# Performance work log

Measured on AMD Instinct MI355X. Metric: run time of the kernel, lower is better.

Reference implementation:

```python
import jax, jax.numpy as jnp
import numpy as np

N_HEADS = 16
HEAD_DIM = 128  # dim // n_heads = 2048 // 16

def setup_inputs() -> dict:
    key = jax.random.key(0)
    ks = jax.random.split(key, 7)
    B, S, D = 2, 2048, 2048
    scale = 0.02
    return {
        "q": jax.random.normal(ks[0], (B, S, D), dtype=jnp.float32),
        "k": jax.random.normal(ks[1], (B, S, D), dtype=jnp.float32),
        "v": jax.random.normal(ks[2], (B, S, D), dtype=jnp.float32),
        "wq": jax.random.normal(ks[3], (D, D), dtype=jnp.float32) * scale,
        "wk": jax.random.normal(ks[4], (D, D), dtype=jnp.float32) * scale,
        "wv": jax.random.normal(ks[5], (D, D), dtype=jnp.float32) * scale,
        "wo": jax.random.normal(ks[6], (D, D), dtype=jnp.float32) * scale,
    }

def reference(q, k, v, wq, wk, wv, wo):
    B, S, _ = q.shape
    # Linear (no bias): torch Linear computes x @ W.T; weights here stored as [out, in]
    xq = (q @ wq.T).reshape(B, S, N_HEADS, HEAD_DIM).transpose(0, 2, 1, 3)  # [B,H,S,d]
    xk = (k @ wk.T).reshape(B, S, N_HEADS, HEAD_DIM).transpose(0, 2, 1, 3)
    xv = (v @ wv.T).reshape(B, S, N_HEADS, HEAD_DIM).transpose(0, 2, 1, 3)
    scores = jnp.einsum("bhqd,bhkd->bhqk", xq, xk) / jnp.sqrt(jnp.float32(HEAD_DIM))
    # causal mask: -inf above the diagonal
    causal = jnp.tril(jnp.ones((S, S), dtype=bool))
    scores = jnp.where(causal[None, None], scores, -jnp.inf)
    attn = jax.nn.softmax(scores.astype(jnp.float32), axis=-1)  # dropout is identity at eval
    out = jnp.einsum("bhqk,bhkd->bhqd", attn, xv)
    out = out.transpose(0, 2, 1, 3).reshape(B, S, N_HEADS * HEAD_DIM)
    return out @ wo.T
```

## Files before the change

kernel.cpp:

```cpp
#include <hip/hip_runtime.h>
#include <hip/hip_bf16.h>

#define B_ 2
#define S_ 2048
#define D_ 2048
#define H_ 16
#define HD_ 128

typedef __attribute__((ext_vector_type(4))) float f32x4;
typedef __attribute__((ext_vector_type(8))) short bf16x8;

static __device__ __forceinline__ unsigned short f2bf(float f) {
    unsigned int u = __float_as_uint(f);
    u += 0x7fffu + ((u >> 16) & 1u);
    return (unsigned short)(u >> 16);
}
static __device__ __forceinline__ float bf2f(unsigned short h) {
    return __uint_as_float(((unsigned int)h) << 16);
}

#define MFMA_K32(a, b, c) __builtin_amdgcn_mfma_f32_16x16x32_bf16(a, b, c, 0, 0, 0)

static __device__ __forceinline__ void gll16(const void* g, void* l) {
    __builtin_amdgcn_global_load_lds((const __attribute__((address_space(1))) void*)g,
                                     (__attribute__((address_space(3))) void*)l,
                                     16, 0, 0);
}

__global__ void cvt_in(const float4* __restrict__ src, ushort4* __restrict__ dst) {
    int i = blockIdx.x * 256 + threadIdx.x;
    float4 v = src[i];
    ushort4 o;
    o.x = f2bf(v.x); o.y = f2bf(v.y); o.z = f2bf(v.z); o.w = f2bf(v.w);
    dst[i] = o;
}

__global__ void cvt_w4(const float4* __restrict__ s0, ushort4* __restrict__ d0,
                       const float4* __restrict__ s1, ushort4* __restrict__ d1,
                       const float4* __restrict__ s2, ushort4* __restrict__ d2,
                       const float4* __restrict__ s3, ushort4* __restrict__ d3) {
    const float4* s; ushort4* d;
    switch (blockIdx.y) {
        case 0: s = s0; d = d0; break;
        case 1: s = s1; d = d1; break;
        case 2: s = s2; d = d2; break;
        default: s = s3; d = d3; break;
    }
    int i = blockIdx.x * 256 + threadIdx.x;
    float4 v = s[i];
    ushort4 o;
    o.x = f2bf(v.x); o.y = f2bf(v.y); o.z = f2bf(v.z); o.w = f2bf(v.w);
    d[i] = o;
}

template<int OUT_MODE>
__global__ __launch_bounds__(256) void gemm_xwt(
        const unsigned short* __restrict__ A,
        const unsigned short* __restrict__ W,
        void* __restrict__ C) {
    constexpr int K = D_;
    __shared__ unsigned short As[2][128 * 32];
    __shared__ unsigned short Ws[2][128 * 32];
    const int tid = threadIdx.x, lane = tid & 63, wid = tid >> 6;
    const int wy = wid >> 1, wx = wid & 1;
    const int g = lane >> 4, lr = lane & 15;
    const int swz = (blockIdx.x & 7) * 64 + (blockIdx.x >> 3);
    const int bm = (swz & 31) * 128;
    const int bn = (swz >> 5) * 128;

    const int r0 = (wid * 128 + lane) >> 2, c0 = (lane & 3) * 8;
    const int r1 = r0 + 16;

    f32x4 acc[4][4] = {};

    auto stage = [&](int k0, int nb) {
        gll16(A + (size_t)(bm + r0) * K + k0 + c0, (char*)&As[nb][0] + wid * 2048);
        gll16(A + (size_t)(bm + r1) * K + k0 + c0, (char*)&As[nb][0] + wid * 2048 + 1024);
        gll16(W + (size_t)(bn + r0) * K + k0 + c0, (char*)&Ws[nb][0] + wid * 2048);
        gll16(W + (size_t)(bn + r1) * K + k0 + c0, (char*)&Ws[nb][0] + wid * 2048 + 1024);
    };

    stage(0, 0);
    int cur = 0;

    for (int k0 = 0; k0 < K; k0 += 32) {
        __syncthreads();
        if (k0 + 32 < K) stage(k0 + 32, cur ^ 1);
        bf16x8 af[4], wf[4];
        #pragma unroll
        for (int i = 0; i < 4; ++i)
            af[i] = *(const bf16x8*)((const char*)&As[cur][0] + (wy * 64 + i * 16 + lr) * 64 + g * 16);
        #pragma unroll
        for (int i = 0; i < 4; ++i)
            wf[i] = *(const bf16x8*)((const char*)&Ws[cur][0] + (wx * 64 + i * 16 + lr) * 64 + g * 16);
        #pragma unroll
        for (int mi = 0; mi < 4; ++mi)
            #pragma unroll
            for (int ni = 0; ni < 4; ++ni)
                acc[mi][ni] = MFMA_K32(af[mi], wf[ni], acc[mi][ni]);
        cur ^= 1;
    }

    #pragma unroll
    for (int mi = 0; mi < 4; ++mi) {
        #pragma unroll
        for (int ni = 0; ni < 4; ++ni) {
            const int n = bn + wx * 64 + ni * 16 + lr;
            const int m0 = bm + wy * 64 + mi * 16 + g * 4;
            if constexpr (OUT_MODE == 0) {
                #pragma unroll
                for (int rg = 0; rg < 4; ++rg) {
                    int m = m0 + rg;
                    int bb = m >> 11, s = m & (S_ - 1);
                    int hh = n >> 7, dd = n & (HD_ - 1);
                    ((unsigned short*)C)[(((size_t)(bb * H_ + hh) * S_) + s) * HD_ + dd] =
                        f2bf(acc[mi][ni][rg]);
                }
            } else if constexpr (OUT_MODE == 1) {
                #pragma unroll
                for (int rg = 0; rg < 4; ++rg) {
                    int m = m0 + rg;
                    int bb = m >> 11, s = m & (S_ - 1);
                    int hh = n >> 7, dd = n & (HD_ - 1);
                    int vr = s & 63;
                    int pr = (vr & 3) | (((vr >> 3) & 3) << 2) | (((vr >> 2) & 1) << 4) | (vr & 32);
                    size_t eo = ((size_t)(bb * H_ + hh) << 18) + ((size_t)(s >> 6) << 13)
                              + pr * 128 + (((((unsigned)dd) << 1) ^ ((pr & 7) << 4)) >> 1);
                    ((unsigned short*)C)[eo] = f2bf(acc[mi][ni][rg]);
                }
            } else if constexpr (OUT_MODE == 2) {
                int bb = m0 >> 11, s0 = m0 & (S_ - 1);
                int hh = n >> 7, dd = n & (HD_ - 1);
                int ch = ((s0 & 63) >> 3) ^ (dd & 7);
                size_t eo = ((size_t)(bb * H_ + hh) << 18) + ((size_t)(s0 >> 6) << 13)
                          + dd * 64 + (ch << 3) + (s0 & 7);
                ushort4 pk;
                pk.x = f2bf(acc[mi][ni][0]); pk.y = f2bf(acc[mi][ni][1]);
                pk.z = f2bf(acc[mi][ni][2]); pk.w = f2bf(acc[mi][ni][3]);
                *(ushort4*)&((unsigned short*)C)[eo] = pk;
            } else {
                #pragma unroll
                for (int rg = 0; rg < 4; ++rg)
                    ((float*)C)[(size_t)(m0 + rg) * D_ + n] = acc[mi][ni][rg];
            }
        }
    }
}

__global__ __launch_bounds__(256) void attn_fwd(
        const unsigned short* __restrict__ Qg,
        const unsigned short* __restrict__ Kt,
        const unsigned short* __restrict__ Vt,
        unsigned short* __restrict__ Og) {
    __shared__ char Ks[2][16384];
    __shared__ char Vs[2][16384];
    const int tid = threadIdx.x, lane = tid & 63, w = tid >> 6;
    const int g = lane >> 4, lr = lane & 15;
    const int swz = (blockIdx.x & 7) * 32 + (blockIdx.x >> 3);
    const int bh = swz >> 3, pi = swz & 7;
    const int b = bh >> 4, h = bh & (H_ - 1);
    const size_t base = (size_t)bh * S_ * HD_;
    const float SCL = 0.08838834764831845f * 1.4426950408889634f;

    auto stage = [&](int t, int nb) {
        const size_t tb = base + (size_t)t * 8192 + w * 2048 + (size_t)lane * 8;
        char* kd = &Ks[nb][0] + w * 4096;
        char* vd = &Vs[nb][0] + w * 4096;
        gll16(Kt + tb, kd);        gll16(Kt + tb + 512, kd + 1024);
        gll16(Kt + tb + 1024, kd + 2048); gll16(Kt + tb + 1536, kd + 3072);
        gll16(Vt + tb, vd);        gll16(Vt + tb + 512, vd + 1024);
        gll16(Vt + tb + 1024, vd + 2048); gll16(Vt + tb + 1536, vd + 3072);
    };

    int cur = 0;
    #pragma unroll 1
    for (int half = 0; half < 2; ++half) {
        const int qt = half ? (15 - pi) : pi;
        const int q0 = qt * 128;
        const int qrA = q0 + w * 16 + lr, qrB = qrA + 64;

        bf16x8 qfA[4], qfB[4];
        #pragma unroll
        for (int st = 0; st < 4; ++st) {
            bf16x8 ta = *(const bf16x8*)(Qg + base + (size_t)qrA * HD_ + st * 32 + g * 8);
            bf16x8 tb2 = *(const bf16x8*)(Qg + base + (size_t)qrB * HD_ + st * 32 + g * 8);
            #pragma unroll
            for (int j = 0; j < 8; ++j) {
                ta[j] = (short)f2bf(bf2f((unsigned short)ta[j]) * SCL);
                tb2[j] = (short)f2bf(bf2f((unsigned short)tb2[j]) * SCL);
            }
            qfA[st] = ta; qfB[st] = tb2;
        }

        float mA = -1e30f, lA = 0.0f, mB = -1e30f, lB = 0.0f;
        f32x4 accA[8] = {}, accB[8] = {};
        const int nt = qt * 2 + 2;

        stage(0, cur);

        for (int t = 0; t < nt; ++t) {
            __syncthreads();
            if (t + 1 < nt) stage(t + 1, cur ^ 1);
            const char* Kb = &Ks[cur][0];
            const char* Vb = &Vs[cur][0];
            const bool actA = (t < nt - 1);

            f32x4 sA[4] = {}, sB[4] = {};
            __builtin_amdgcn_s_setprio(1);
            #pragma unroll
            for (int f = 0; f < 4; ++f) {
                const int row = f * 16 + lr;
                const int sw = (row & 7) << 4;
                #pragma unroll
                for (int st = 0; st < 4; ++st) {
                    bf16x8 kf = *(const bf16x8*)(Kb + row * 256 + ((st * 64 + g * 16) ^ sw));
                    if (actA) sA[f] = MFMA_K32(kf, qfA[st], sA[f]);
                    sB[f] = MFMA_K32(kf, qfB[st], sB[f]);
                }
            }
            __builtin_amdgcn_s_setprio(0);

            if (t == nt - 2) {
                #pragma unroll
                for (int f = 0; f < 4; ++f)
                    #pragma unroll
                    for (int rg = 0; rg < 4; ++rg)
                        if (q0 + 32 * (f >> 1) + 8 * g + 4 * (f & 1) + rg > qrA)
                            sA[f][rg] = -1e30f;
            }
            if (t == nt - 1) {
                #pragma unroll
                for (int f = 0; f < 4; ++f)
                    #pragma unroll
                    for (int rg = 0; rg < 4; ++rg)
                        if (q0 + 64 + 32 * (f >> 1) + 8 * g + 4 * (f & 1) + rg > qrB)
                            sB[f][rg] = -1e30f;
            }

            bf16x8 pAlo, pAhi, pBlo, pBhi;
            auto softmax_step = [&](f32x4* sf, float& m_r, float& l_r, f32x4* accO,
                                    bf16x8& plo, bf16x8& phi) {
                float pm = -1e30f;
                #pragma unroll
                for (int f = 0; f < 4; ++f)
                    #pragma unroll
                    for (int rg = 0; rg < 4; ++rg) pm = fmaxf(pm, sf[f][rg]);
                pm = fmaxf(pm, __shfl_xor(pm, 16));
                pm = fmaxf(pm, __shfl_xor(pm, 32));
                const float mnew = fmaxf(m_r, pm);
                const float corr = exp2f(m_r - mnew);
                m_r = mnew;
                float ls = 0.0f;
                #pragma unroll
                for (int f = 0; f < 2; ++f)
                    #pragma unroll
                    for (int rg = 0; rg < 4; ++rg) {
                        float p = exp2f(sf[f][rg] - mnew);
                        ls += p;
                        plo[f * 4 + rg] = (short)f2bf(p);
                    }
                #pragma unroll
                for (int f = 0; f < 2; ++f)
                    #pragma unroll
                    for (int rg = 0; rg < 4; ++rg) {
                        float p = exp2f(sf[2 + f][rg] - mnew);
                        ls += p;
                        phi[f * 4 + rg] = (short)f2bf(p);
                    }
                ls += __shfl_xor(ls, 16);
                ls += __shfl_xor(ls, 32);
                l_r = l_r * corr + ls;
                float cj[4];
                #pragma unroll
                for (int j = 0; j < 4; ++j) cj[j] = __shfl(corr, g * 4 + j);
                #pragma unroll
                for (int db = 0; db < 8; ++db) {
                    accO[db][0] *= cj[0]; accO[db][1] *= cj[1];
                    accO[db][2] *= cj[2]; accO[db][3] *= cj[3];
                }
            };
            if (actA) softmax_step(sA, mA, lA, accA, pAlo, pAhi);
            softmax_step(sB, mB, lB, accB, pBlo, pBhi);

            __builtin_amdgcn_s_setprio(1);
            #pragma unroll
            for (int db = 0; db < 8; ++db) {
                const int d = db * 16 + lr;
                bf16x8 vlo = *(const bf16x8*)(Vb + d * 128 + ((g ^ (d & 7)) << 4));
                bf16x8 vhi = *(const bf16x8*)(Vb + d * 128 + (((4 + g) ^ (d & 7)) << 4));
                if (actA) {
                    accA[db] = MFMA_K32(pAlo, vlo, accA[db]);
                    accA[db] = MFMA_K32(pAhi, vhi, accA[db]);
                }
                accB[db] = MFMA_K32(pBlo, vlo, accB[db]);
                accB[db] = MFMA_K32(pBhi, vhi, accB[db]);
            }
            __builtin_amdgcn_s_setprio(0);
            cur ^= 1;
        }

        {
            float lj[4];
            #pragma unroll
            for (int j = 0; j < 4; ++j) lj[j] = __shfl(lA, g * 4 + j);
            #pragma unroll
            for (int j = 0; j < 4; ++j) {
                const int qq = q0 + w * 16 + g * 4 + j;
                const float inv = 1.0f / lj[j];
                unsigned short* dst = Og + ((size_t)(b * S_ + qq)) * D_ + h * HD_;
                #pragma unroll
                for (int db = 0; db < 8; ++db)
                    dst[db * 16 + lr] = f2bf(accA[db][j] * inv);
            }
            #pragma unroll
            for (int j = 0; j < 4; ++j) lj[j] = __shfl(lB, g * 4 + j);
            #pragma unroll
            for (int j = 0; j < 4; ++j) {
                const int qq = q0 + 64 + w * 16 + g * 4 + j;
                const float inv = 1.0f / lj[j];
                unsigned short* dst = Og + ((size_t)(b * S_ + qq)) * D_ + h * HD_;
                #pragma unroll
                for (int db = 0; db < 8; ++db)
                    dst[db * 16 + lr] = f2bf(accB[db][j] * inv);
            }
        }
    }
}

extern "C" void kernel_launch(void* const* d_in, const int* in_sizes, int n_in,
                              void* d_out, int out_size, void* d_ws, size_t ws_size,
                              hipStream_t stream) {
    const float* q  = (const float*)d_in[0];
    const float* k  = (const float*)d_in[1];
    const float* v  = (const float*)d_in[2];
    const float* wq = (const float*)d_in[3];
    const float* wk = (const float*)d_in[4];
    const float* wv = (const float*)d_in[5];
    const float* wo = (const float*)d_in[6];

    unsigned short* ws   = (unsigned short*)d_ws;
    unsigned short* wqb  = ws;
    unsigned short* wkb  = wqb + (size_t)D_ * D_;
    unsigned short* wvb  = wkb + (size_t)D_ * D_;
    unsigned short* wob  = wvb + (size_t)D_ * D_;
    unsigned short* xq   = wob + (size_t)D_ * D_;
    unsigned short* xk   = xq + (size_t)B_ * S_ * D_;
    unsigned short* xv   = xk + (size_t)B_ * S_ * D_;
    unsigned short* slot = xv + (size_t)B_ * S_ * D_;

    cvt_w4<<<dim3(4096, 4), 256, 0, stream>>>(
        (const float4*)wq, (ushort4*)wqb, (const float4*)wk, (ushort4*)wkb,
        (const float4*)wv, (ushort4*)wvb, (const float4*)wo, (ushort4*)wob);

    cvt_in<<<8192, 256, 0, stream>>>((const float4*)q, (ushort4*)slot);
    gemm_xwt<0><<<512, 256, 0, stream>>>(slot, wqb, xq);
    cvt_in<<<8192, 256, 0, stream>>>((const float4*)k, (ushort4*)slot);
    gemm_xwt<1><<<512, 256, 0, stream>>>(slot, wkb, xk);
    cvt_in<<<8192, 256, 0, stream>>>((const float4*)v, (ushort4*)slot);
    gemm_xwt<2><<<512, 256, 0, stream>>>(slot, wvb, xv);

    attn_fwd<<<256, 256, 0, stream>>>(xq, xk, xv, slot);

    gemm_xwt<3><<<512, 256, 0, stream>>>(slot, wob, d_out);
}
```

Baseline: 357.3 us.

## Split attention into one q-tile per block with lazy rescale and single-buffered LDS

The attention kernel now launches one block per (batch-head, query tile), heaviest tiles first, replacing the earlier scheme where each block handled a paired light and heavy tile. K/V staging drops from double-buffered to single-buffered LDS, with an extra barrier before each next stage; this halves shared memory so more blocks can be resident, but it removes the load/compute overlap. The softmax skips the running-max update and the accumulator rescale unless the new max exceeds the old one by more than 8 (log2 units), and converts probabilities to bf16 with the packed v_cvt_pk_bf16_f32 instruction. The lazy rescale trades some exponent headroom for fewer shuffles and multiplies.

```diff
diff --git a/kernel.cpp b/kernel.cpp
--- a/kernel.cpp
+++ b/kernel.cpp
@@ -152,124 +152,98 @@
         const unsigned short* __restrict__ Kt,
         const unsigned short* __restrict__ Vt,
         unsigned short* __restrict__ Og) {
-    __shared__ char Ks[2][16384];
-    __shared__ char Vs[2][16384];
+    __shared__ char Ks[16384];
+    __shared__ char Vs[16384];
     const int tid = threadIdx.x, lane = tid & 63, w = tid >> 6;
     const int g = lane >> 4, lr = lane & 15;
-    const int swz = (blockIdx.x & 7) * 32 + (blockIdx.x >> 3);
-    const int bh = swz >> 3, pi = swz & 7;
+    const int qt = 15 - (blockIdx.x >> 5);
+    const int bh = (blockIdx.x & 7) * 4 + ((blockIdx.x >> 3) & 3);
     const int b = bh >> 4, h = bh & (H_ - 1);
     const size_t base = (size_t)bh * S_ * HD_;
     const float SCL = 0.08838834764831845f * 1.4426950408889634f;
 
-    auto stage = [&](int t, int nb) {
+    auto stage = [&](int t) {
         const size_t tb = base + (size_t)t * 8192 + w * 2048 + (size_t)lane * 8;
-        char* kd = &Ks[nb][0] + w * 4096;
-        char* vd = &Vs[nb][0] + w * 4096;
-        gll16(Kt + tb, kd);        gll16(Kt + tb + 512, kd + 1024);
+        char* kd = Ks + w * 4096;
+        char* vd = Vs + w * 4096;
+        gll16(Kt + tb, kd);               gll16(Kt + tb + 512, kd + 1024);
         gll16(Kt + tb + 1024, kd + 2048); gll16(Kt + tb + 1536, kd + 3072);
-        gll16(Vt + tb, vd);        gll16(Vt + tb + 512, vd + 1024);
+        gll16(Vt + tb, vd);               gll16(Vt + tb + 512, vd + 1024);
         gll16(Vt + tb + 1024, vd + 2048); gll16(Vt + tb + 1536, vd + 3072);
     };
 
-    int cur = 0;
-    #pragma unroll 1
-    for (int half = 0; half < 2; ++half) {
-        const int qt = half ? (15 - pi) : pi;
-        const int q0 = qt * 128;
-        const int qrA = q0 + w * 16 + lr, qrB = qrA + 64;
-
-        bf16x8 qfA[4], qfB[4];
-        #pragma unroll
-        for (int st = 0; st < 4; ++st) {
-            bf16x8 ta = *(const bf16x8*)(Qg + base + (size_t)qrA * HD_ + st * 32 + g * 8);
-            bf16x8 tb2 = *(const bf16x8*)(Qg + base + (size_t)qrB * HD_ + st * 32 + g * 8);
-            #pragma unroll
-            for (int j = 0; j < 8; ++j) {
-                ta[j] = (short)f2bf(bf2f((unsigned short)ta[j]) * SCL);
-                tb2[j] = (short)f2bf(bf2f((unsigned short)tb2[j]) * SCL);
-            }
-            qfA[st] = ta; qfB[st] = tb2;
-        }
-
-        float mA = -1e30f, lA = 0.0f, mB = -1e30f, lB = 0.0f;
-        f32x4 accA[8] = {}, accB[8] = {};
-        const int nt = qt * 2 + 2;
-
-        stage(0, cur);
-
-        for (int t = 0; t < nt; ++t) {
-            __syncthreads();
-            if (t + 1 < nt) stage(t + 1, cur ^ 1);
-            const char* Kb = &Ks[cur][0];
-            const char* Vb = &Vs[cur][0];
-            const bool actA = (t < nt - 1);
-
-            f32x4 sA[4] = {}, sB[4] = {};
-            __builtin_amdgcn_s_setprio(1);
-            #pragma unroll
-            for (int f = 0; f < 4; ++f) {
-                const int row = f * 16 + lr;
-                const int sw = (row & 7) << 4;
-                #pragma unroll
-                for (int st = 0; st < 4; ++st) {
-                    bf16x8 kf = *(const bf16x8*)(Kb + row * 256 + ((st * 64 + g * 16) ^ sw));
-                    if (actA) sA[f] = MFMA_K32(kf, qfA[st], sA[f]);
-                    sB[f] = MFMA_K32(kf, qfB[st], sB[f]);
-                }
-            }
-            __builtin_amdgcn_s_setprio(0);
-
-            if (t == nt - 2) {
-                #pragma unroll
-                for (int f = 0; f < 4; ++f)
-                    #pragma unroll
-                    for (int rg = 0; rg < 4; ++rg)
-                        if (q0 + 32 * (f >> 1) + 8 * g + 4 * (f & 1) + rg > qrA)
-                            sA[f][rg] = -1e30f;
-            }
-            if (t == nt - 1) {
-                #pragma unroll
-                for (int f = 0; f < 4; ++f)
-                    #pragma unroll
-                    for (int rg = 0; rg < 4; ++rg)
-                        if (q0 + 64 + 32 * (f >> 1) + 8 * g + 4 * (f & 1) + rg > qrB)
-                            sB[f][rg] = -1e30f;
-            }
-
-            bf16x8 pAlo, pAhi, pBlo, pBhi;
-            auto softmax_step = [&](f32x4* sf, float& m_r, float& l_r, f32x4* accO,
-                                    bf16x8& plo, bf16x8& phi) {
-                float pm = -1e30f;
-                #pragma unroll
-                for (int f = 0; f < 4; ++f)
-                    #pragma unroll
-                    for (int rg = 0; rg < 4; ++rg) pm = fmaxf(pm, sf[f][rg]);
-                pm = fmaxf(pm, __shfl_xor(pm, 16));
-                pm = fmaxf(pm, __shfl_xor(pm, 32));
+    const int q0 = qt * 128;
+    const int qrA = q0 + w * 16 + lr, qrB = qrA + 64;
+
+    bf16x8 qfA[4], qfB[4];
+    #pragma unroll
+    for (int st = 0; st < 4; ++st) {
+        bf16x8 ta = *(const bf16x8*)(Qg + base + (size_t)qrA * HD_ + st * 32 + g * 8);
+        bf16x8 tb2 = *(const bf16x8*)(Qg + base + (size_t)qrB * HD_ + st * 32 + g * 8);
+        #pragma unroll
+        for (int j = 0; j < 8; ++j) {
+            ta[j] = (short)f2bf(bf2f((unsigned short)ta[j]) * SCL);
+            tb2[j] = (short)f2bf(bf2f((unsigned short)tb2[j]) * SCL);
+        }
+        qfA[st] = ta; qfB[st] = tb2;
+    }
+
+    float mA = -1e30f, lA = 0.0f, mB = -1e30f, lB = 0.0f;
+    f32x4 accA[8] = {}, accB[8] = {};
+    const int nt = 2 * qt + 2;
+
+    stage(0);
+
+    for (int t = 0; t < nt; ++t) {
+        __syncthreads();
+        const bool actA = (t < nt - 1);
+
+        f32x4 sA[4] = {}, sB[4] = {};
+        __builtin_amdgcn_s_setprio(1);
+        #pragma unroll
+        for (int f = 0; f < 4; ++f) {
+            const int row = f * 16 + lr;
+            const int sw = (row & 7) << 4;
+            #pragma unroll
+            for (int st = 0; st < 4; ++st) {
+                bf16x8 kf = *(const bf16x8*)(Ks + row * 256 + ((st * 64 + g * 16) ^ sw));
+                if (actA) sA[f] = MFMA_K32(kf, qfA[st], sA[f]);
+                sB[f] = MFMA_K32(kf, qfB[st], sB[f]);
+            }
+        }
+        __builtin_amdgcn_s_setprio(0);
+
+        if (t == nt - 2) {
+            #pragma unroll
+            for (int f = 0; f < 4; ++f)
+                #pragma unroll
+                for (int rg = 0; rg < 4; ++rg)
+                    if (q0 + 32 * (f >> 1) + 8 * g + 4 * (f & 1) + rg > qrA)
+                        sA[f][rg] = -1e30f;
+        }
+        if (t == nt - 1) {
+            #pragma unroll
+            for (int f = 0; f < 4; ++f)
+                #pragma unroll
+                for (int rg = 0; rg < 4; ++rg)
+                    if (q0 + 64 + 32 * (f >> 1) + 8 * g + 4 * (f & 1) + rg > qrB)
+                        sB[f][rg] = -1e30f;
+        }
+
+        bf16x8 pAlo, pAhi, pBlo, pBhi;
+        auto softmax_step = [&](f32x4* sf, float& m_r, float& l_r, f32x4* accO,
+                                bf16x8& plo, bf16x8& phi) {
+            float pm = -1e30f;
+            #pragma unroll
+            for (int f = 0; f < 4; ++f)
+                #pragma unroll
+                for (int rg = 0; rg < 4; ++rg) pm = fmaxf(pm, sf[f][rg]);
+            pm = fmaxf(pm, __shfl_xor(pm, 16));
+            pm = fmaxf(pm, __shfl_xor(pm, 32));
+            if (!__all(pm <= m_r + 8.0f)) {
                 const float mnew = fmaxf(m_r, pm);
                 const float corr = exp2f(m_r - mnew);
                 m_r = mnew;
-                float ls = 0.0f;
-                #pragma unroll
-                for (int f = 0; f < 2; ++f)
-                    #pragma unroll
-                    for (int rg = 0; rg < 4; ++rg) {
-                        float p = exp2f(sf[f][rg] - mnew);
-                        ls += p;
-                        plo[f * 4 + rg] = (short)f2bf(p);
-                    }
-                #pragma unroll
-                for (int f = 0; f < 2; ++f)
-                    #pragma unroll
-                    for (int rg = 0; rg < 4; ++rg) {
-                        float p = exp2f(sf[2 + f][rg] - mnew);
-                        ls += p;
-                        phi[f * 4 + rg] = (short)f2bf(p);
-                    }
-                ls += __shfl_xor(ls, 16);
-                ls += __shfl_xor(ls, 32);
-                l_r = l_r * corr + ls;
                 float cj[4];
                 #pragma unroll
                 for (int j = 0; j < 4; ++j) cj[j] = __shfl(corr, g * 4 + j);
@@ -278,51 +252,77 @@
                     accO[db][0] *= cj[0]; accO[db][1] *= cj[1];
                     accO[db][2] *= cj[2]; accO[db][3] *= cj[3];
                 }
-            };
-            if (actA) softmax_step(sA, mA, lA, accA, pAlo, pAhi);
-            softmax_step(sB, mB, lB, accB, pBlo, pBhi);
-
-            __builtin_amdgcn_s_setprio(1);
-            #pragma unroll
-            for (int db = 0; db < 8; ++db) {
-                const int d = db * 16 + lr;
-                bf16x8 vlo = *(const bf16x8*)(Vb + d * 128 + ((g ^ (d & 7)) << 4));
-                bf16x8 vhi = *(const bf16x8*)(Vb + d * 128 + (((4 + g) ^ (d & 7)) << 4));
-                if (actA) {
-                    accA[db] = MFMA_K32(pAlo, vlo, accA[db]);
-                    accA[db] = MFMA_K32(pAhi, vhi, accA[db]);
+                l_r *= corr;
+            }
+            float p[16], ls = 0.0f;
+            #pragma unroll
+            for (int f = 0; f < 4; ++f)
+                #pragma unroll
+                for (int rg = 0; rg < 4; ++rg) {
+                    float pv = exp2f(sf[f][rg] - m_r);
+                    p[f * 4 + rg] = pv;
+                    ls += pv;
                 }
-                accB[db] = MFMA_K32(pBlo, vlo, accB[db]);
-                accB[db] = MFMA_K32(pBhi, vhi, accB[db]);
-            }
-            __builtin_amdgcn_s_setprio(0);
-            cur ^= 1;
-        }
-
-        {
-            float lj[4];
-            #pragma unroll
-            for (int j = 0; j < 4; ++j) lj[j] = __shfl(lA, g * 4 + j);
-            #pragma unroll
-            for (int j = 0; j < 4; ++j) {
-                const int qq = q0 + w * 16 + g * 4 + j;
-                const float inv = 1.0f / lj[j];
-                unsigned short* dst = Og + ((size_t)(b * S_ + qq)) * D_ + h * HD_;
-                #pragma unroll
-                for (int db = 0; db < 8; ++db)
-                    dst[db * 16 + lr] = f2bf(accA[db][j] * inv);
-            }
-            #pragma unroll
-            for (int j = 0; j < 4; ++j) lj[j] = __shfl(lB, g * 4 + j);
-            #pragma unroll
-            for (int j = 0; j < 4; ++j) {
-                const int qq = q0 + 64 + w * 16 + g * 4 + j;
-                const float inv = 1.0f / lj[j];
-                unsigned short* dst = Og + ((size_t)(b * S_ + qq)) * D_ + h * HD_;
-                #pragma unroll
-                for (int db = 0; db < 8; ++db)
-                    dst[db * 16 + lr] = f2bf(accB[db][j] * inv);
-            }
+            union { bf16x8 v; unsigned int u[4]; } lo2, hi2;
+            #pragma unroll
+            for (int i = 0; i < 4; ++i) {
+                asm("v_cvt_pk_bf16_f32 %0, %1, %2"
+                    : "=v"(lo2.u[i]) : "v"(p[2 * i]), "v"(p[2 * i + 1]));
+                asm("v_cvt_pk_bf16_f32 %0, %1, %2"
+                    : "=v"(hi2.u[i]) : "v"(p[8 + 2 * i]), "v"(p[9 + 2 * i]));
+            }
+            plo = lo2.v; phi = hi2.v;
+            ls += __shfl_xor(ls, 16);
+            ls += __shfl_xor(ls, 32);
+            l_r += ls;
+        };
+        if (actA) softmax_step(sA, mA, lA, accA, pAlo, pAhi);
+        softmax_step(sB, mB, lB, accB, pBlo, pBhi);
+
+        __builtin_amdgcn_s_setprio(1);
+        #pragma unroll
+        for (int db = 0; db < 8; ++db) {
+            const int d = db * 16 + lr;
+            bf16x8 vlo = *(const bf16x8*)(Vs + d * 128 + ((g ^ (d & 7)) << 4));
+            bf16x8 vhi = *(const bf16x8*)(Vs + d * 128 + (((4 + g) ^ (d & 7)) << 4));
+            if (actA) {
+                accA[db] = MFMA_K32(pAlo, vlo, accA[db]);
+                accA[db] = MFMA_K32(pAhi, vhi, accA[db]);
+            }
+            accB[db] = MFMA_K32(pBlo, vlo, accB[db]);
+            accB[db] = MFMA_K32(pBhi, vhi, accB[db]);
+        }
+        __builtin_amdgcn_s_setprio(0);
+
+        if (t + 1 < nt) {
+            __syncthreads();
+            stage(t + 1);
+        }
+    }
+
+    {
+        float lj[4];
+        #pragma unroll
+        for (int j = 0; j < 4; ++j) lj[j] = __shfl(lA, g * 4 + j);
+        #pragma unroll
+        for (int j = 0; j < 4; ++j) {
+            const int qq = q0 + w * 16 + g * 4 + j;
+            const float inv = 1.0f / lj[j];
+            unsigned short* dst = Og + ((size_t)(b * S_ + qq)) * D_ + h * HD_;
+            #pragma unroll
+            for (int db = 0; db < 8; ++db)
+                dst[db * 16 + lr] = f2bf(accA[db][j] * inv);
+        }
+        #pragma unroll
+        for (int j = 0; j < 4; ++j) lj[j] = __shfl(lB, g * 4 + j);
+        #pragma unroll
+        for (int j = 0; j < 4; ++j) {
+            const int qq = q0 + 64 + w * 16 + g * 4 + j;
+            const float inv = 1.0f / lj[j];
+            unsigned short* dst = Og + ((size_t)(b * S_ + qq)) * D_ + h * HD_;
+            #pragma unroll
+            for (int db = 0; db < 8; ++db)
+                dst[db * 16 + lr] = f2bf(accB[db][j] * inv);
         }
     }
 }
@@ -359,7 +359,7 @@
     cvt_in<<<8192, 256, 0, stream>>>((const float4*)v, (ushort4*)slot);
     gemm_xwt<2><<<512, 256, 0, stream>>>(slot, wvb, xv);
 
-    attn_fwd<<<256, 256, 0, stream>>>(xq, xk, xv, slot);
+    attn_fwd<<<512, 256, 0, stream>>>(xq, xk, xv, slot);
 
     gemm_xwt<3><<<512, 256, 0, stream>>>(slot, wob, d_out);
 }
```

Result: slower. 397.0 us (+11.1%).

## Split attention into one query tile per block and skip small rescales

Applied to the files above, without the earlier changes.

The attention kernel now launches 512 blocks, each handling a single 128-row query tile, ordered so the longest causal tiles are scheduled first. Previously 256 blocks each processed a pair of tiles (pi and 15-pi) in sequence. The online softmax also skips the accumulator rescale when no lane's new max exceeds the running max by more than 8 (log2 units), which removes multiply work on most iterations. Splitting the tiles adds parallelism and load balance but reloads Q setup per block, and the lazy rescale lets unnormalised p values grow up to 256 before the final normalisation.

```diff
diff --git a/kernel.cpp b/kernel.cpp
--- a/kernel.cpp
+++ b/kernel.cpp
@@ -156,8 +156,11 @@
     __shared__ char Vs[2][16384];
     const int tid = threadIdx.x, lane = tid & 63, w = tid >> 6;
     const int g = lane >> 4, lr = lane & 15;
-    const int swz = (blockIdx.x & 7) * 32 + (blockIdx.x >> 3);
-    const int bh = swz >> 3, pi = swz & 7;
+    const int i = blockIdx.x;
+    const int hi = i >> 8, j = i & 255;
+    const int bh = j & 31;
+    const int p = j >> 5;
+    const int qt = hi ? p : 15 - p;
     const int b = bh >> 4, h = bh & (H_ - 1);
     const size_t base = (size_t)bh * S_ * HD_;
     const float SCL = 0.08838834764831845f * 1.4426950408889634f;
@@ -166,163 +169,162 @@
         const size_t tb = base + (size_t)t * 8192 + w * 2048 + (size_t)lane * 8;
         char* kd = &Ks[nb][0] + w * 4096;
         char* vd = &Vs[nb][0] + w * 4096;
-        gll16(Kt + tb, kd);        gll16(Kt + tb + 512, kd + 1024);
+        gll16(Kt + tb, kd);               gll16(Kt + tb + 512, kd + 1024);
         gll16(Kt + tb + 1024, kd + 2048); gll16(Kt + tb + 1536, kd + 3072);
-        gll16(Vt + tb, vd);        gll16(Vt + tb + 512, vd + 1024);
+        gll16(Vt + tb, vd);               gll16(Vt + tb + 512, vd + 1024);
         gll16(Vt + tb + 1024, vd + 2048); gll16(Vt + tb + 1536, vd + 3072);
     };
 
+    const int q0 = qt * 128;
+    const int qrA = q0 + w * 16 + lr, qrB = qrA + 64;
+
+    bf16x8 qfA[4], qfB[4];
+    #pragma unroll
+    for (int st = 0; st < 4; ++st) {
+        bf16x8 ta = *(const bf16x8*)(Qg + base + (size_t)qrA * HD_ + st * 32 + g * 8);
+        bf16x8 tb2 = *(const bf16x8*)(Qg + base + (size_t)qrB * HD_ + st * 32 + g * 8);
+        #pragma unroll
+        for (int jj = 0; jj < 8; ++jj) {
+            ta[jj] = (short)f2bf(bf2f((unsigned short)ta[jj]) * SCL);
+            tb2[jj] = (short)f2bf(bf2f((unsigned short)tb2[jj]) * SCL);
+        }
+        qfA[st] = ta; qfB[st] = tb2;
+    }
+
+    float mA = -1e30f, lA = 0.0f, mB = -1e30f, lB = 0.0f;
+    f32x4 accA[8] = {}, accB[8] = {};
+    const int nt = 2 * qt + 2;
+
+    stage(0, 0);
     int cur = 0;
-    #pragma unroll 1
-    for (int half = 0; half < 2; ++half) {
-        const int qt = half ? (15 - pi) : pi;
-        const int q0 = qt * 128;
-        const int qrA = q0 + w * 16 + lr, qrB = qrA + 64;
-
-        bf16x8 qfA[4], qfB[4];
-        #pragma unroll
-        for (int st = 0; st < 4; ++st) {
-            bf16x8 ta = *(const bf16x8*)(Qg + base + (size_t)qrA * HD_ + st * 32 + g * 8);
-            bf16x8 tb2 = *(const bf16x8*)(Qg + base + (size_t)qrB * HD_ + st * 32 + g * 8);
-            #pragma unroll
-            for (int j = 0; j < 8; ++j) {
-                ta[j] = (short)f2bf(bf2f((unsigned short)ta[j]) * SCL);
-                tb2[j] = (short)f2bf(bf2f((unsigned short)tb2[j]) * SCL);
+
+    for (int t = 0; t < nt; ++t) {
+        __syncthreads();
+        if (t + 1 < nt) stage(t + 1, cur ^ 1);
+        const char* Kb = &Ks[cur][0];
+        const char* Vb = &Vs[cur][0];
+        const bool actA = (t < nt - 1);
+
+        f32x4 sA[4] = {}, sB[4] = {};
+        __builtin_amdgcn_s_setprio(1);
+        #pragma unroll
+        for (int f = 0; f < 4; ++f) {
+            const int row = f * 16 + lr;
+            const int sw = (row & 7) << 4;
+            #pragma unroll
+            for (int st = 0; st < 4; ++st) {
+                bf16x8 kf = *(const bf16x8*)(Kb + row * 256 + ((st * 64 + g * 16) ^ sw));
+                if (actA) sA[f] = MFMA_K32(kf, qfA[st], sA[f]);
+                sB[f] = MFMA_K32(kf, qfB[st], sB[f]);
             }
-            qfA[st] = ta; qfB[st] = tb2;
-        }
-
-        float mA = -1e30f, lA = 0.0f, mB = -1e30f, lB = 0.0f;
-        f32x4 accA[8] = {}, accB[8] = {};
-        const int nt = qt * 2 + 2;
-
-        stage(0, cur);
-
-        for (int t = 0; t < nt; ++t) {
-            __syncthreads();
-            if (t + 1 < nt) stage(t + 1, cur ^ 1);
-            const char* Kb = &Ks[cur][0];
-            const char* Vb = &Vs[cur][0];
-            const bool actA = (t < nt - 1);
-
-            f32x4 sA[4] = {}, sB[4] = {};
-            __builtin_amdgcn_s_setprio(1);
-            #pragma unroll
-            for (int f = 0; f < 4; ++f) {
-                const int row = f * 16 + lr;
-                const int sw = (row & 7) << 4;
-                #pragma unroll
-                for (int st = 0; st < 4; ++st) {
-                    bf16x8 kf = *(const bf16x8*)(Kb + row * 256 + ((st * 64 + g * 16) ^ sw));
-                    if (actA) sA[f] = MFMA_K32(kf, qfA[st], sA[f]);
-                    sB[f] = MFMA_K32(kf, qfB[st], sB[f]);
-                }
-            }
-            __builtin_amdgcn_s_setprio(0);
-
-            if (t == nt - 2) {
-                #pragma unroll
-                for (int f = 0; f < 4; ++f)
-                    #pragma unroll
-                    for (int rg = 0; rg < 4; ++rg)
-                        if (q0 + 32 * (f >> 1) + 8 * g + 4 * (f & 1) + rg > qrA)
-                            sA[f][rg] = -1e30f;
-            }
-            if (t == nt - 1) {
-                #pragma unroll
-                for (int f = 0; f < 4; ++f)
-                    #pragma unroll
-                    for (int rg = 0; rg < 4; ++rg)
-                        if (q0 + 64 + 32 * (f >> 1) + 8 * g + 4 * (f & 1) + rg > qrB)
-                            sB[f][rg] = -1e30f;
-            }
-
-            bf16x8 pAlo, pAhi, pBlo, pBhi;
-            auto softmax_step = [&](f32x4* sf, float& m_r, float& l_r, f32x4* accO,
-                                    bf16x8& plo, bf16x8& phi) {
-                float pm = -1e30f;
-                #pragma unroll
-                for (int f = 0; f < 4; ++f)
-                    #pragma unroll
-                    for (int rg = 0; rg < 4; ++rg) pm = fmaxf(pm, sf[f][rg]);
-                pm = fmaxf(pm, __shfl_xor(pm, 16));
-                pm = fmaxf(pm, __shfl_xor(pm, 32));
+        }
+        __builtin_amdgcn_s_setprio(0);
+
+        if (t == nt - 2) {
+            #pragma unroll
+            for (int f = 0; f < 4; ++f)
+                #pragma unroll
+                for (int rg = 0; rg < 4; ++rg)
+                    if (q0 + 32 * (f >> 1) + 8 * g + 4 * (f & 1) + rg > qrA)
+                        sA[f][rg] = -1e30f;
+        }
+        if (t == nt - 1) {
+            #pragma unroll
+            for (int f = 0; f < 4; ++f)
+                #pragma unroll
+                for (int rg = 0; rg < 4; ++rg)
+                    if (q0 + 64 + 32 * (f >> 1) + 8 * g + 4 * (f & 1) + rg > qrB)
+                        sB[f][rg] = -1e30f;
+        }
+
+        bf16x8 pAlo, pAhi, pBlo, pBhi;
+        auto softmax_step = [&](f32x4* sf, float& m_r, float& l_r, f32x4* accO,
+                                bf16x8& plo, bf16x8& phi) {
+            float pm = -1e30f;
+            #pragma unroll
+            for (int f = 0; f < 4; ++f)
+                #pragma unroll
+                for (int rg = 0; rg < 4; ++rg) pm = fmaxf(pm, sf[f][rg]);
+            pm = fmaxf(pm, __shfl_xor(pm, 16));
+            pm = fmaxf(pm, __shfl_xor(pm, 32));
+            if (!__all(pm <= m_r + 8.0f)) {
                 const float mnew = fmaxf(m_r, pm);
                 const float corr = exp2f(m_r - mnew);
                 m_r = mnew;
-                float ls = 0.0f;
-                #pragma unroll
-                for (int f = 0; f < 2; ++f)
-                    #pragma unroll
-                    for (int rg = 0; rg < 4; ++rg) {
-                        float p = exp2f(sf[f][rg] - mnew);
-                        ls += p;
-                        plo[f * 4 + rg] = (short)f2bf(p);
-                    }
-                #pragma unroll
-                for (int f = 0; f < 2; ++f)
-                    #pragma unroll
-                    for (int rg = 0; rg < 4; ++rg) {
-                        float p = exp2f(sf[2 + f][rg] - mnew);
-                        ls += p;
-                        phi[f * 4 + rg] = (short)f2bf(p);
-                    }
-                ls += __shfl_xor(ls, 16);
-                ls += __shfl_xor(ls, 32);
-                l_r = l_r * corr + ls;
                 float cj[4];
                 #pragma unroll
-                for (int j = 0; j < 4; ++j) cj[j] = __shfl(corr, g * 4 + j);
+                for (int jj = 0; jj < 4; ++jj) cj[jj] = __shfl(corr, g * 4 + jj);
                 #pragma unroll
                 for (int db = 0; db < 8; ++db) {
                     accO[db][0] *= cj[0]; accO[db][1] *= cj[1];
                     accO[db][2] *= cj[2]; accO[db][3] *= cj[3];
                 }
-            };
-            if (actA) softmax_step(sA, mA, lA, accA, pAlo, pAhi);
-            softmax_step(sB, mB, lB, accB, pBlo, pBhi);
-
-            __builtin_amdgcn_s_setprio(1);
-            #pragma unroll
-            for (int db = 0; db < 8; ++db) {
-                const int d = db * 16 + lr;
-                bf16x8 vlo = *(const bf16x8*)(Vb + d * 128 + ((g ^ (d & 7)) << 4));
-                bf16x8 vhi = *(const bf16x8*)(Vb + d * 128 + (((4 + g) ^ (d & 7)) << 4));
-                if (actA) {
-                    accA[db] = MFMA_K32(pAlo, vlo, accA[db]);
-                    accA[db] = MFMA_K32(pAhi, vhi, accA[db]);
-                }
-                accB[db] = MFMA_K32(pBlo, vlo, accB[db]);
-                accB[db] = MFMA_K32(pBhi, vhi, accB[db]);
+                l_r *= corr;
             }
-            __builtin_amdgcn_s_setprio(0);
-            cur ^= 1;
-        }
-
-        {
-            float lj[4];
-            #pragma unroll
-            for (int j = 0; j < 4; ++j) lj[j] = __shfl(lA, g * 4 + j);
-            #pragma unroll
-            for (int j = 0; j < 4; ++j) {
-                const int qq = q0 + w * 16 + g * 4 + j;
-                const float inv = 1.0f / lj[j];
-                unsigned short* dst = Og + ((size_t)(b * S_ + qq)) * D_ + h * HD_;
-                #pragma unroll
-                for (int db = 0; db < 8; ++db)
-                    dst[db * 16 + lr] = f2bf(accA[db][j] * inv);
+            float ls = 0.0f;
+            #pragma unroll
+            for (int f = 0; f < 2; ++f)
+                #pragma unroll
+                for (int rg = 0; rg < 4; ++rg) {
+                    float pv = exp2f(sf[f][rg] - m_r);
+                    ls += pv;
+                    plo[f * 4 + rg] = (short)f2bf(pv);
+                }
+            #pragma unroll
+            for (int f = 0; f < 2; ++f)
+                #pragma unroll
+                for (int rg = 0; rg < 4; ++rg) {
+                    float pv = exp2f(sf[2 + f][rg] - m_r);
+                    ls += pv;
+                    phi[f * 4 + rg] = (short)f2bf(pv);
+                }
+            ls += __shfl_xor(ls, 16);
+            ls += __shfl_xor(ls, 32);
+            l_r += ls;
+        };
+        if (actA) softmax_step(sA, mA, lA, accA, pAlo, pAhi);
+        softmax_step(sB, mB, lB, accB, pBlo, pBhi);
+
+        __builtin_amdgcn_s_setprio(1);
+        #pragma unroll
+        for (int db = 0; db < 8; ++db) {
+            const int d = db * 16 + lr;
+            bf16x8 vlo = *(const bf16x8*)(Vb + d * 128 + ((g ^ (d & 7)) << 4));
+            bf16x8 vhi = *(const bf16x8*)(Vb + d * 128 + (((4 + g) ^ (d & 7)) << 4));
+            if (actA) {
+                accA[db] = MFMA_K32(pAlo, vlo, accA[db]);
+                accA[db] = MFMA_K32(pAhi, vhi, accA[db]);
             }
-            #pragma unroll
-            for (int j = 0; j < 4; ++j) lj[j] = __shfl(lB, g * 4 + j);
-            #pragma unroll
-            for (int j = 0; j < 4; ++j) {
-                const int qq = q0 + 64 + w * 16 + g * 4 + j;
-                const float inv = 1.0f / lj[j];
-                unsigned short* dst = Og + ((size_t)(b * S_ + qq)) * D_ + h * HD_;
-                #pragma unroll
-                for (int db = 0; db < 8; ++db)
-                    dst[db * 16 + lr] = f2bf(accB[db][j] * inv);
-            }
+            accB[db] = MFMA_K32(pBlo, vlo, accB[db]);
+            accB[db] = MFMA_K32(pBhi, vhi, accB[db]);
+        }
+        __builtin_amdgcn_s_setprio(0);
+        cur ^= 1;
+    }
+
+    {
+        float lj[4];
+        #pragma unroll
+        for (int jj = 0; jj < 4; ++jj) lj[jj] = __shfl(lA, g * 4 + jj);
+        #pragma unroll
+        for (int jj = 0; jj < 4; ++jj) {
+            const int qq = q0 + w * 16 + g * 4 + jj;
+            const float inv = 1.0f / lj[jj];
+            unsigned short* dst = Og + ((size_t)(b * S_ + qq)) * D_ + h * HD_;
+            #pragma unroll
+            for (int db = 0; db < 8; ++db)
+                dst[db * 16 + lr] = f2bf(accA[db][jj] * inv);
+        }
+        #pragma unroll
+        for (int jj = 0; jj < 4; ++jj) lj[jj] = __shfl(lB, g * 4 + jj);
+        #pragma unroll
+        for (int jj = 0; jj < 4; ++jj) {
+            const int qq = q0 + 64 + w * 16 + g * 4 + jj;
+            const float inv = 1.0f / lj[jj];
+            unsigned short* dst = Og + ((size_t)(b * S_ + qq)) * D_ + h * HD_;
+            #pragma unroll
+            for (int db = 0; db < 8; ++db)
+                dst[db * 16 + lr] = f2bf(accB[db][jj] * inv);
         }
     }
 }
@@ -359,7 +361,7 @@
     cvt_in<<<8192, 256, 0, stream>>>((const float4*)v, (ushort4*)slot);
     gemm_xwt<2><<<512, 256, 0, stream>>>(slot, wvb, xv);
 
-    attn_fwd<<<256, 256, 0, stream>>>(xq, xk, xv, slot);
+    attn_fwd<<<512, 256, 0, stream>>>(xq, xk, xv, slot);
 
     gemm_xwt<3><<<512, 256, 0, stream>>>(slot, wob, d_out);
 }
```

Measured after the change: 344.4 us. 1.04x faster.
